# Kernel optimization log

Hardware: AMD Instinct MI355X
Metric: run time of the kernel (lower is better)

## Reference

```python
import jax, jax.numpy as jnp
import numpy as np

B, IN, HID, H = 8192, 1024, 2048, 8
UP = 2 * IN          # input_size * proj_factor
HS = HID // H        # head size = 256
EPS = 1e-5


def _blockdiag(x, w, b):
    # x: [B, UP] -> chunk into H blocks of UP//H, per-block linear to HID//H
    xb = x.reshape(B, H, UP // H)
    y = jnp.einsum('bhi,hio->bho', xb, w)
    return y.reshape(B, HID) + b


def setup_inputs() -> dict:
    key = jax.random.key(0)
    ks = jax.random.split(key, 20)
    rn = lambda k, s: jax.random.normal(k, s, jnp.float32)
    p = lambda k, *s: rn(k, s) * 0.02
    return dict(
        x=rn(ks[0], (B, IN)),
        h_prev=rn(ks[1], (B, HID)), c_prev=rn(ks[2], (B, HID)),
        n_prev=rn(ks[3], (B, HID)), m_prev=rn(ks[4], (B, HID)),
        ln_g=jnp.ones(IN), ln_b=jnp.zeros(IN),
        w_ul=p(ks[5], IN, UP), b_ul=jnp.zeros(UP),
        w_ur=p(ks[6], IN, HID), b_ur=jnp.zeros(HID),
        conv_w=p(ks[7], 4), conv_b=jnp.zeros(()),
        w_skip=p(ks[8], UP, HID), b_skip=jnp.zeros(HID),
        w_q=p(ks[9], H, UP // H, HID // H), b_q=jnp.zeros(HID),
        w_k=p(ks[10], H, UP // H, HID // H), b_k=jnp.zeros(HID),
        w_v=p(ks[11], H, UP // H, HID // H), b_v=jnp.zeros(HID),
        w_i=p(ks[12], UP, HID), b_i=jnp.zeros(HID),
        w_f=p(ks[13], UP, HID), b_f=jnp.zeros(HID),
        w_o=p(ks[14], UP, HID), b_o=jnp.zeros(HID),
        gn_g=jnp.ones(HID), gn_b=jnp.zeros(HID),
        w_down=p(ks[15], HID, IN), b_down=jnp.zeros(IN),
    )


def reference(x, h_prev, c_prev, n_prev, m_prev, ln_g, ln_b,
              w_ul, b_ul, w_ur, b_ur, conv_w, conv_b, w_skip, b_skip,
              w_q, b_q, w_k, b_k, w_v, b_v, w_i, b_i, w_f, b_f, w_o, b_o,
              gn_g, gn_b, w_down, b_down):
    # LayerNorm over features
    mu = x.mean(-1, keepdims=True)
    var = x.var(-1, keepdims=True)
    xn = (x - mu) * jax.lax.rsqrt(var + EPS) * ln_g + ln_b

    xul = xn @ w_ul + b_ul          # [B, UP]
    xur = xn @ w_ur + b_ur          # [B, HID]

    # causal conv1d (kernel 4, 1 channel) along the feature axis, left-pad 3
    xp = jnp.pad(xul, ((0, 0), (3, 0)))
    xc = conv_b + sum(conv_w[j] * xp[:, j:j + UP] for j in range(4))
    xc = jax.nn.silu(xc)            # [B, UP]

    x_skip = xc @ w_skip + b_skip

    q = _blockdiag(xc, w_q, b_q)
    k = _blockdiag(xc, w_k, b_k) / np.sqrt(HS).astype(np.float32)
    v = _blockdiag(xul, w_v, b_v)

    i_t = xc @ w_i + b_i
    f_t = xc @ w_f + b_f
    o = jax.nn.sigmoid(xul @ w_o + b_o)

    m_t = jnp.maximum(f_t + m_prev, i_t)
    i = jnp.exp(i_t - m_t)
    f = jnp.exp(f_t + m_prev - m_t)
    c_t = f * c_prev + i * (v * k)
    n_t = f * n_prev + i * k

    denom = jnp.max(jnp.abs(n_t.T @ q), axis=1)     # [HID]
    h_t = o * (c_t * q) / denom

    # GroupNorm on (N, C), groups = H
    hg = h_t.reshape(B, H, HID // H)
    gm = hg.mean(-1, keepdims=True)
    gv = hg.var(-1, keepdims=True)
    hn = ((hg - gm) * jax.lax.rsqrt(gv + EPS)).reshape(B, HID) * gn_g + gn_b

    out = (hn + x_skip) * jax.nn.silu(xur)
    return out @ w_down + b_down + x, h_t, c_t, n_t, m_t
```

## Files before the change

kernel.cpp:

```cpp
#include <hip/hip_runtime.h>
#include <stdint.h>

#define B_    8192
#define IN_   1024
#define HID_  2048
#define UP_   2048
#define H_    8
#define HS_   256
#define EPS_  1e-5f

typedef __bf16 bf16x8 __attribute__((ext_vector_type(8)));
typedef float f32x4 __attribute__((ext_vector_type(4)));
typedef unsigned short u16x4 __attribute__((ext_vector_type(4)));
typedef unsigned short u16x8 __attribute__((ext_vector_type(8)));

__device__ __forceinline__ unsigned short f2bf(float f) {
  union { float f; unsigned int u; } v; v.f = f;
  unsigned int u = v.u;
  unsigned int r = (u + 0x7fffu + ((u >> 16) & 1u)) >> 16;
  return (unsigned short)r;
}
__device__ __forceinline__ float bf2f(unsigned short h) {
  union { unsigned int u; float f; } v; v.u = ((unsigned int)h) << 16;
  return v.f;
}

__device__ __forceinline__ void gload_lds16(const void* g, void* l) {
  auto gp = reinterpret_cast<const uint32_t __attribute__((address_space(1)))*>(
      reinterpret_cast<uintptr_t>(g));
  auto lp = reinterpret_cast<uint32_t __attribute__((address_space(3)))*>(
      reinterpret_cast<uintptr_t>(l));
  __builtin_amdgcn_global_load_lds(gp, lp, 16, 0, 0);
}

template <typename OutT, bool HAS_ADD>
__global__ __launch_bounds__(512, 2) void gemm8p(
    const unsigned short* __restrict__ A, int lda, int a_zoff,
    const unsigned short* __restrict__ W, int ldw, int w_zoff,
    const float* __restrict__ bias, int bias_zoff,
    OutT* __restrict__ C, int ldc, int c_zoff,
    const float* __restrict__ ADD, float scale, int K)
{
  __shared__ char lds[131072];
  const int z = blockIdx.z;
  A += (size_t)z * a_zoff;
  W += (size_t)z * w_zoff;
  if (bias) bias += (size_t)z * bias_zoff;

  const int nwg = gridDim.x * gridDim.y;
  const int orig = blockIdx.y * gridDim.x + blockIdx.x;
  const int q8 = nwg >> 3, r8 = nwg & 7;
  const int xcd = orig & 7, xi = orig >> 3;
  const int wg = (xcd < r8 ? xcd * (q8 + 1) : r8 * (q8 + 1) + (xcd - r8) * q8) + xi;
  const int bx = wg % gridDim.x, by = wg / gridDim.x;

  const int t = threadIdx.x;
  const int lane = t & 63, wave = t >> 6;
  const int wr = wave >> 2, wc = wave & 3;
  const int l15 = lane & 15, l4 = lane >> 4;
  const int row0 = by * 256, col0 = bx * 256;

  const int lrow = lane >> 3;
  const int lslot = (lane & 7) ^ lrow;
  const size_t aLane = (size_t)lrow * lda * 2 + (size_t)lslot * 16;
  const size_t wLane = (size_t)lrow * ldw * 2 + (size_t)lslot * 16;
  const char* Abase = (const char*)A;
  const char* Wbase = (const char*)W;

  const int aRdBase = (wr * 128 + l15) * 128 + (((l4) ^ (l15 & 7)) * 16);
  const int bRdBase = (wc * 64 + l15) * 128 + (((l4) ^ (l15 & 7)) * 16);

  auto issueA = [&](int buf, int half, int tile) {
#pragma unroll
    for (int j = 0; j < 2; ++j) {
      const int rbase = half * 128 + j * 64 + wave * 8;
      gload_lds16(Abase + (size_t)(row0 + rbase) * (lda * 2) + (size_t)tile * 128 + aLane,
                  lds + buf * 65536 + rbase * 128 + lane * 16);
    }
  };
  auto issueB = [&](int buf, int half, int tile) {
#pragma unroll
    for (int j = 0; j < 2; ++j) {
      const int rbase = half * 128 + j * 64 + wave * 8;
      gload_lds16(Wbase + (size_t)(col0 + rbase) * (ldw * 2) + (size_t)tile * 128 + wLane,
                  lds + buf * 65536 + 32768 + rbase * 128 + lane * 16);
    }
  };

  f32x4 acc[8][4] = {};
  const int NT = K >> 6;

  issueA(0, 0, 0); issueA(0, 1, 0);
  issueB(0, 0, 0); issueB(0, 1, 0);
  issueB(1, 0, 1); issueB(1, 1, 1);
  asm volatile("s_waitcnt vmcnt(4)" ::: "memory");
  __builtin_amdgcn_s_barrier();
  __builtin_amdgcn_sched_barrier(0);

  for (int T = 0; T < NT; ++T) {
    const int buf = T & 1;
    const char* ldsA = lds + buf * 65536;
    const char* ldsB = ldsA + 32768;
    bf16x8 bfr[4][2];
#pragma unroll
    for (int q = 0; q < 4; ++q) {
      if (q == 0) {
#pragma unroll
        for (int ni = 0; ni < 4; ++ni) {
          bfr[ni][0] = *(const bf16x8*)(ldsB + (bRdBase + ni * 2048));
          bfr[ni][1] = *(const bf16x8*)(ldsB + ((bRdBase + ni * 2048) ^ 64));
        }
      }
      bf16x8 af[2][2];
#pragma unroll
      for (int m2 = 0; m2 < 2; ++m2) {
        const int mi = q * 2 + m2;
        af[m2][0] = *(const bf16x8*)(ldsA + (aRdBase + mi * 2048));
        af[m2][1] = *(const bf16x8*)(ldsA + ((aRdBase + mi * 2048) ^ 64));
      }
      if (q == 0 && T + 1 < NT) issueA(buf ^ 1, 0, T + 1);
      if (q == 1 && T + 1 < NT) issueA(buf ^ 1, 1, T + 1);
      if (q == 2 && T + 2 < NT) issueB(buf, 0, T + 2);
      if (q == 3 && T + 2 < NT) issueB(buf, 1, T + 2);
      if (q == 0) asm volatile("s_waitcnt lgkmcnt(8)" ::: "memory");
      __builtin_amdgcn_s_barrier();
      asm volatile("s_waitcnt lgkmcnt(0)" ::: "memory");
      __builtin_amdgcn_sched_barrier(0);
      __builtin_amdgcn_s_setprio(1);
#pragma unroll
      for (int kq = 0; kq < 2; ++kq)
#pragma unroll
        for (int m2 = 0; m2 < 2; ++m2)
#pragma unroll
          for (int ni = 0; ni < 4; ++ni)
            acc[q * 2 + m2][ni] = __builtin_amdgcn_mfma_f32_16x16x32_bf16(
                af[m2][kq], bfr[ni][kq], acc[q * 2 + m2][ni], 0, 0, 0);
      __builtin_amdgcn_s_setprio(0);
      if (q == 3) {
        if (T + 2 < NT) asm volatile("s_waitcnt vmcnt(4)" ::: "memory");
        else            asm volatile("s_waitcnt vmcnt(0)" ::: "memory");
      }
      __builtin_amdgcn_s_barrier();
      __builtin_amdgcn_sched_barrier(0);
    }
  }

#pragma unroll
  for (int mi = 0; mi < 8; ++mi) {
#pragma unroll
    for (int ni = 0; ni < 4; ++ni) {
#pragma unroll
      for (int r = 0; r < 4; ++r) {
        const int m = row0 + wr * 128 + mi * 16 + l4 * 4 + r;
        const int n = wc * 64 + ni * 16 + l15;
        float v = acc[mi][ni][r];
        if (bias) v += bias[col0 + n];
        v *= scale;
        const size_t ci = (size_t)m * ldc + (size_t)z * c_zoff + col0 + n;
        if constexpr (HAS_ADD) v += ADD[ci];
        if constexpr (sizeof(OutT) == 2) C[ci] = (OutT)f2bf(v);
        else C[ci] = v;
      }
    }
  }
}

__global__ __launch_bounds__(256) void denom_reduce(
    const float* __restrict__ part, float* __restrict__ denom)
{
  const int m = blockIdx.x, t = threadIdx.x;
  const size_t P = (size_t)HID_ * HID_;
  float v = 0.f;
  for (int n = t; n < HID_; n += 256) {
    const size_t o = (size_t)m * HID_ + n;
    float s = part[o] + part[P + o] + part[2 * P + o] + part[3 * P + o];
    v = fmaxf(v, fabsf(s));
  }
#pragma unroll
  for (int off = 1; off < 64; off <<= 1) v = fmaxf(v, __shfl_xor(v, off, 64));
  __shared__ float red[4];
  if ((t & 63) == 0) red[t >> 6] = v;
  __syncthreads();
  if (t == 0) denom[m] = fmaxf(fmaxf(red[0], red[1]), fmaxf(red[2], red[3]));
}

template <typename InT>
__global__ __launch_bounds__(256) void transpose_bf(
    const InT* __restrict__ in, unsigned short* __restrict__ out, int R, int C)
{
  __shared__ float tile[32][33];
  const size_t zoff = (size_t)blockIdx.z * R * C;
  in += zoff; out += zoff;
  const int cb = blockIdx.x * 32, rb = blockIdx.y * 32;
  const int tx = threadIdx.x, ty = threadIdx.y;
  for (int i = ty; i < 32; i += 8) {
    InT v = in[(size_t)(rb + i) * C + cb + tx];
    float f;
    if constexpr (sizeof(InT) == 2) f = bf2f((unsigned short)v);
    else f = (float)v;
    tile[i][tx] = f;
  }
  __syncthreads();
  for (int i = ty; i < 32; i += 8)
    out[(size_t)(cb + i) * R + rb + tx] = f2bf(tile[tx][i]);
}

__global__ __launch_bounds__(256) void ln_kernel(
    const float* __restrict__ x, const float* __restrict__ g,
    const float* __restrict__ b, unsigned short* __restrict__ xn)
{
  const int brow = blockIdx.x, t = threadIdx.x;
  const int lane = t & 63, wave = t >> 6;
  const float* xr = x + (size_t)brow * IN_;
  f32x4 v = *(const f32x4*)(xr + t * 4);
  float s = v[0] + v[1] + v[2] + v[3];
  float q = v[0]*v[0] + v[1]*v[1] + v[2]*v[2] + v[3]*v[3];
#pragma unroll
  for (int off = 32; off; off >>= 1) {
    s += __shfl_xor(s, off, 64);
    q += __shfl_xor(q, off, 64);
  }
  __shared__ float ss[4], sq[4];
  if (lane == 0) { ss[wave] = s; sq[wave] = q; }
  __syncthreads();
  s = ss[0] + ss[1] + ss[2] + ss[3];
  q = sq[0] + sq[1] + sq[2] + sq[3];
  const float mean = s * (1.f / IN_);
  const float var = q * (1.f / IN_) - mean * mean;
  const float rs = rsqrtf(var + EPS_);
  u16x4 o;
#pragma unroll
  for (int e = 0; e < 4; ++e) {
    const int j = t * 4 + e;
    o[e] = f2bf((v[e] - mean) * rs * g[j] + b[j]);
  }
  *(u16x4*)(xn + (size_t)brow * IN_ + t * 4) = o;
}

__global__ __launch_bounds__(256) void conv_kernel(
    const unsigned short* __restrict__ xul, const float* __restrict__ cw,
    const float* __restrict__ cb, unsigned short* __restrict__ xc)
{
  const int brow = blockIdx.x, t = threadIdx.x;
  const size_t base = (size_t)brow * UP_;
  const int j0 = t * 8;
  float xv[11];
#pragma unroll
  for (int e = 0; e < 11; ++e) {
    const int j = j0 + e - 3;
    xv[e] = (j >= 0) ? bf2f(xul[base + j]) : 0.f;
  }
  const float w0 = cw[0], w1 = cw[1], w2 = cw[2], w3 = cw[3], bb = cb[0];
  u16x8 o;
#pragma unroll
  for (int e = 0; e < 8; ++e) {
    float sv = bb + w0 * xv[e] + w1 * xv[e + 1] + w2 * xv[e + 2] + w3 * xv[e + 3];
    o[e] = f2bf(sv / (1.f + expf(-sv)));
  }
  *(u16x8*)(xc + base + j0) = o;
}

__global__ __launch_bounds__(256) void gates_kernel(
    const float* __restrict__ it_, const float* __restrict__ ft_,
    const unsigned short* __restrict__ kb, const unsigned short* __restrict__ vb,
    const float* __restrict__ mprev, const float* __restrict__ cprev,
    const float* __restrict__ nprev,
    float* __restrict__ mo, float* __restrict__ co, float* __restrict__ no)
{
  const size_t idx = ((size_t)blockIdx.x * 256 + threadIdx.x) * 4;
  f32x4 iv = *(const f32x4*)(it_ + idx);
  f32x4 fv = *(const f32x4*)(ft_ + idx);
  f32x4 mp = *(const f32x4*)(mprev + idx);
  f32x4 cp = *(const f32x4*)(cprev + idx);
  f32x4 np = *(const f32x4*)(nprev + idx);
  u16x4 kv = *(const u16x4*)(kb + idx);
  u16x4 vv = *(const u16x4*)(vb + idx);
  f32x4 mo4, co4, no4;
#pragma unroll
  for (int e = 0; e < 4; ++e) {
    const float ft = fv[e] + mp[e];
    const float mt = fmaxf(ft, iv[e]);
    const float ie = expf(iv[e] - mt);
    const float fe = expf(ft - mt);
    const float k = bf2f(kv[e]), v = bf2f(vv[e]);
    mo4[e] = mt;
    co4[e] = fe * cp[e] + ie * (v * k);
    no4[e] = fe * np[e] + ie * k;
  }
  *(f32x4*)(mo + idx) = mo4;
  *(f32x4*)(co + idx) = co4;
  *(f32x4*)(no + idx) = no4;
}

__global__ __launch_bounds__(256) void hgn_kernel(
    const float* __restrict__ ct, const unsigned short* __restrict__ olin,
    const unsigned short* __restrict__ qb, const float* __restrict__ denom,
    const unsigned short* __restrict__ skipb, const unsigned short* __restrict__ xurb,
    const float* __restrict__ gng, const float* __restrict__ gnb,
    float* __restrict__ ho, unsigned short* __restrict__ pre)
{
  const int brow = blockIdx.x, t = threadIdx.x;
  const size_t base = (size_t)brow * HID_ + t * 8;
  u16x8 ov = *(const u16x8*)(olin + base);
  u16x8 qv = *(const u16x8*)(qb + base);
  f32x4 c0 = *(const f32x4*)(ct + base);
  f32x4 c1 = *(const f32x4*)(ct + base + 4);
  float h[8];
  float s = 0.f, sq = 0.f;
#pragma unroll
  for (int e = 0; e < 8; ++e) {
    const float o = 1.f / (1.f + expf(-bf2f(ov[e])));
    const float cv = (e < 4) ? c0[e] : c1[e - 4];
    const float hv = o * cv * bf2f(qv[e]) / denom[t * 8 + e];
    h[e] = hv; s += hv; sq += hv * hv;
  }
#pragma unroll
  for (int e = 0; e < 8; ++e) ho[base + e] = h[e];
#pragma unroll
  for (int off = 1; off < 32; off <<= 1) {
    s += __shfl_xor(s, off, 64);
    sq += __shfl_xor(sq, off, 64);
  }
  const float mean = s * (1.f / HS_);
  const float var = sq * (1.f / HS_) - mean * mean;
  const float rs = rsqrtf(var + EPS_);
  u16x8 sv = *(const u16x8*)(skipb + base);
  u16x8 xv = *(const u16x8*)(xurb + base);
  u16x8 pv;
#pragma unroll
  for (int e = 0; e < 8; ++e) {
    const int j = t * 8 + e;
    const float hn = (h[e] - mean) * rs * gng[j] + gnb[j];
    const float xr = bf2f(xv[e]);
    const float sil = xr / (1.f + expf(-xr));
    pv[e] = f2bf((hn + bf2f(sv[e])) * sil);
  }
  *(u16x8*)(pre + base) = pv;
}

extern "C" void kernel_launch(void* const* d_in, const int* in_sizes, int n_in,
                              void* d_out, int out_size, void* d_ws, size_t ws_size,
                              hipStream_t stream)
{
  const float* x      = (const float*)d_in[0];
  const float* c_prev = (const float*)d_in[2];
  const float* n_prev = (const float*)d_in[3];
  const float* m_prev = (const float*)d_in[4];
  const float* ln_g   = (const float*)d_in[5];
  const float* ln_b   = (const float*)d_in[6];
  const float* w_ul   = (const float*)d_in[7];
  const float* b_ul   = (const float*)d_in[8];
  const float* w_ur   = (const float*)d_in[9];
  const float* b_ur   = (const float*)d_in[10];
  const float* conv_w = (const float*)d_in[11];
  const float* conv_b = (const float*)d_in[12];
  const float* w_skip = (const float*)d_in[13];
  const float* b_skip = (const float*)d_in[14];
  const float* w_q    = (const float*)d_in[15];
  const float* b_q    = (const float*)d_in[16];
  const float* w_k    = (const float*)d_in[17];
  const float* b_k    = (const float*)d_in[18];
  const float* w_v    = (const float*)d_in[19];
  const float* b_v    = (const float*)d_in[20];
  const float* w_i    = (const float*)d_in[21];
  const float* b_i    = (const float*)d_in[22];
  const float* w_f    = (const float*)d_in[23];
  const float* b_f    = (const float*)d_in[24];
  const float* w_o    = (const float*)d_in[25];
  const float* b_o    = (const float*)d_in[26];
  const float* gn_g   = (const float*)d_in[27];
  const float* gn_b   = (const float*)d_in[28];
  const float* w_down = (const float*)d_in[29];
  const float* b_down = (const float*)d_in[30];

  float* out_p = (float*)d_out;
  float* h_p = out_p + (size_t)B_ * IN_;
  float* c_p = h_p + (size_t)B_ * HID_;
  float* n_p = c_p + (size_t)B_ * HID_;
  float* m_p = n_p + (size_t)B_ * HID_;

  char* ws = (char*)d_ws;
  size_t off = 0;
  auto alloc = [&](size_t n) -> void* {
    void* p = ws + off;
    off += (n + 255) & ~(size_t)255;
    return p;
  };

  const size_t BH2 = (size_t)B_ * HID_ * 2;
  const size_t BH4 = (size_t)B_ * HID_ * 4;

  unsigned short* xn_bf   = (unsigned short*)alloc((size_t)B_ * IN_ * 2);
  unsigned short* xul_bf  = (unsigned short*)alloc(BH2);
  unsigned short* xur_bf  = (unsigned short*)alloc(BH2);
  unsigned short* xc_bf   = (unsigned short*)alloc(BH2);
  unsigned short* skip_bf = (unsigned short*)alloc(BH2);
  unsigned short* q_bf    = (unsigned short*)alloc(BH2);
  unsigned short* k_bf    = (unsigned short*)alloc(BH2);
  unsigned short* v_bf    = (unsigned short*)alloc(BH2);
  unsigned short* olin_bf = (unsigned short*)alloc(BH2);
  unsigned short* qT_bf   = (unsigned short*)alloc(BH2);
  unsigned short* nT_bf   = (unsigned short*)alloc(BH2);
  unsigned short* pre_bf  = (unsigned short*)alloc(BH2);
  float* i_f   = (float*)alloc(BH4);
  float* f_f   = (float*)alloc(BH4);
  float* denom = (float*)alloc(HID_ * sizeof(float));
  float* part  = (float*)alloc((size_t)4 * HID_ * HID_ * sizeof(float));
  unsigned short* wt_ul   = (unsigned short*)alloc((size_t)IN_ * UP_ * 2);
  unsigned short* wt_ur   = (unsigned short*)alloc((size_t)IN_ * HID_ * 2);
  unsigned short* wt_skip = (unsigned short*)alloc((size_t)UP_ * HID_ * 2);
  unsigned short* wt_q    = (unsigned short*)alloc((size_t)H_ * HS_ * HS_ * 2);
  unsigned short* wt_k    = (unsigned short*)alloc((size_t)H_ * HS_ * HS_ * 2);
  unsigned short* wt_v    = (unsigned short*)alloc((size_t)H_ * HS_ * HS_ * 2);
  unsigned short* wt_i    = (unsigned short*)alloc((size_t)UP_ * HID_ * 2);
  unsigned short* wt_f    = (unsigned short*)alloc((size_t)UP_ * HID_ * 2);
  unsigned short* wt_o    = (unsigned short*)alloc((size_t)UP_ * HID_ * 2);
  unsigned short* wt_down = (unsigned short*)alloc((size_t)HID_ * IN_ * 2);

  if (off > ws_size) return;

  const dim3 tb32(32, 8);

  transpose_bf<float><<<dim3(64, 32, 1), tb32, 0, stream>>>(w_ul, wt_ul, 1024, 2048);
  transpose_bf<float><<<dim3(64, 32, 1), tb32, 0, stream>>>(w_ur, wt_ur, 1024, 2048);
  transpose_bf<float><<<dim3(64, 64, 1), tb32, 0, stream>>>(w_skip, wt_skip, 2048, 2048);
  transpose_bf<float><<<dim3(8, 8, 8), tb32, 0, stream>>>(w_q, wt_q, 256, 256);
  transpose_bf<float><<<dim3(8, 8, 8), tb32, 0, stream>>>(w_k, wt_k, 256, 256);
  transpose_bf<float><<<dim3(8, 8, 8), tb32, 0, stream>>>(w_v, wt_v, 256, 256);
  transpose_bf<float><<<dim3(64, 64, 1), tb32, 0, stream>>>(w_i, wt_i, 2048, 2048);
  transpose_bf<float><<<dim3(64, 64, 1), tb32, 0, stream>>>(w_f, wt_f, 2048, 2048);
  transpose_bf<float><<<dim3(64, 64, 1), tb32, 0, stream>>>(w_o, wt_o, 2048, 2048);
  transpose_bf<float><<<dim3(32, 64, 1), tb32, 0, stream>>>(w_down, wt_down, 2048, 1024);

  ln_kernel<<<B_, 256, 0, stream>>>(x, ln_g, ln_b, xn_bf);

  gemm8p<unsigned short, false><<<dim3(8, 32, 1), 512, 0, stream>>>(
      xn_bf, IN_, 0, wt_ul, IN_, 0, b_ul, 0, xul_bf, UP_, 0, nullptr, 1.f, IN_);
  gemm8p<unsigned short, false><<<dim3(8, 32, 1), 512, 0, stream>>>(
      xn_bf, IN_, 0, wt_ur, IN_, 0, b_ur, 0, xur_bf, HID_, 0, nullptr, 1.f, IN_);

  conv_kernel<<<B_, 256, 0, stream>>>(xul_bf, conv_w, conv_b, xc_bf);

  gemm8p<unsigned short, false><<<dim3(8, 32, 1), 512, 0, stream>>>(
      xc_bf, UP_, 0, wt_skip, UP_, 0, b_skip, 0, skip_bf, HID_, 0, nullptr, 1.f, UP_);
  gemm8p<unsigned short, false><<<dim3(1, 32, 8), 512, 0, stream>>>(
      xc_bf, UP_, HS_, wt_q, HS_, HS_ * HS_, b_q, HS_, q_bf, HID_, HS_, nullptr, 1.f, HS_);
  gemm8p<unsigned short, false><<<dim3(1, 32, 8), 512, 0, stream>>>(
      xc_bf, UP_, HS_, wt_k, HS_, HS_ * HS_, b_k, HS_, k_bf, HID_, HS_, nullptr, 0.0625f, HS_);
  gemm8p<unsigned short, false><<<dim3(1, 32, 8), 512, 0, stream>>>(
      xul_bf, UP_, HS_, wt_v, HS_, HS_ * HS_, b_v, HS_, v_bf, HID_, HS_, nullptr, 1.f, HS_);
  gemm8p<float, false><<<dim3(8, 32, 1), 512, 0, stream>>>(
      xc_bf, UP_, 0, wt_i, UP_, 0, b_i, 0, i_f, HID_, 0, nullptr, 1.f, UP_);
  gemm8p<float, false><<<dim3(8, 32, 1), 512, 0, stream>>>(
      xc_bf, UP_, 0, wt_f, UP_, 0, b_f, 0, f_f, HID_, 0, nullptr, 1.f, UP_);
  gemm8p<unsigned short, false><<<dim3(8, 32, 1), 512, 0, stream>>>(
      xul_bf, UP_, 0, wt_o, UP_, 0, b_o, 0, olin_bf, HID_, 0, nullptr, 1.f, UP_);

  gates_kernel<<<(B_ * HID_ / 4) / 256, 256, 0, stream>>>(
      i_f, f_f, k_bf, v_bf, m_prev, c_prev, n_prev, m_p, c_p, n_p);

  transpose_bf<unsigned short><<<dim3(64, 256, 1), tb32, 0, stream>>>(q_bf, qT_bf, B_, HID_);
  transpose_bf<float><<<dim3(64, 256, 1), tb32, 0, stream>>>(n_p, nT_bf, B_, HID_);

  gemm8p<float, false><<<dim3(8, 8, 4), 512, 0, stream>>>(
      nT_bf, B_, HID_, qT_bf, B_, HID_, nullptr, 0,
      part, HID_, HID_ * HID_, nullptr, 1.f, B_ / 4);
  denom_reduce<<<HID_, 256, 0, stream>>>(part, denom);

  hgn_kernel<<<B_, 256, 0, stream>>>(
      c_p, olin_bf, q_bf, denom, skip_bf, xur_bf, gn_g, gn_b, h_p, pre_bf);

  gemm8p<float, true><<<dim3(4, 32, 1), 512, 0, stream>>>(
      pre_bf, UP_, 0, wt_down, UP_, 0, b_down, 0, out_p, IN_, 0, x, 1.f, UP_);
}
```

Baseline: 1.039 ms.

## Batch same-input GEMMs into wide GEMMs and fuse n transpose into gates

Several projections that share an input now run as single wider GEMMs: ul/ur share one launch, skip/i/f form one 6144-wide GEMM, and q/k share one launch, with an epilogue that routes output columns to separate buffers, biases and scales. The i and f gate pre-activations are now stored in bf16 instead of fp32, which cuts memory traffic but lowers precision of the exponent inputs. The gates kernel is retiled to 64x64 blocks and writes the transposed bf16 n directly through LDS, removing a separate transpose pass over n. This reduces launches and tail effects and reuses A tiles across the fused outputs.

```diff
diff --git a/kernel.cpp b/kernel.cpp
--- a/kernel.cpp
+++ b/kernel.cpp
@@ -37,15 +37,18 @@
 __global__ __launch_bounds__(512, 2) void gemm8p(
     const unsigned short* __restrict__ A, int lda, int a_zoff,
     const unsigned short* __restrict__ W, int ldw, int w_zoff,
-    const float* __restrict__ bias, int bias_zoff,
-    OutT* __restrict__ C, int ldc, int c_zoff,
-    const float* __restrict__ ADD, float scale, int K)
+    const float* __restrict__ bias, const float* __restrict__ bias2,
+    int bias_zoff,
+    OutT* __restrict__ C, OutT* __restrict__ C2, int ldc, int c_zoff,
+    int c_split,
+    const float* __restrict__ ADD, float scale, float scale2, int K)
 {
   __shared__ char lds[131072];
   const int z = blockIdx.z;
   A += (size_t)z * a_zoff;
   W += (size_t)z * w_zoff;
   if (bias) bias += (size_t)z * bias_zoff;
+  if (bias2) bias2 += (size_t)z * bias_zoff;
 
   const int nwg = gridDim.x * gridDim.y;
   const int orig = blockIdx.y * gridDim.x + blockIdx.x;
@@ -145,6 +148,11 @@
     }
   }
 
+  const float* bp = bias;
+  OutT* Cp = C;
+  int cbase = col0;
+  float sc = scale;
+  if (col0 >= c_split) { bp = bias2; Cp = C2; cbase = col0 - c_split; sc = scale2; }
 #pragma unroll
   for (int mi = 0; mi < 8; ++mi) {
 #pragma unroll
@@ -154,12 +162,12 @@
         const int m = row0 + wr * 128 + mi * 16 + l4 * 4 + r;
         const int n = wc * 64 + ni * 16 + l15;
         float v = acc[mi][ni][r];
-        if (bias) v += bias[col0 + n];
-        v *= scale;
-        const size_t ci = (size_t)m * ldc + (size_t)z * c_zoff + col0 + n;
+        if (bp) v += bp[cbase + n];
+        v *= sc;
+        const size_t ci = (size_t)m * ldc + (size_t)z * c_zoff + cbase + n;
         if constexpr (HAS_ADD) v += ADD[ci];
-        if constexpr (sizeof(OutT) == 2) C[ci] = (OutT)f2bf(v);
-        else C[ci] = v;
+        if constexpr (sizeof(OutT) == 2) Cp[ci] = (OutT)f2bf(v);
+        else Cp[ci] = v;
       }
     }
   }
@@ -186,11 +194,12 @@
 
 template <typename InT>
 __global__ __launch_bounds__(256) void transpose_bf(
-    const InT* __restrict__ in, unsigned short* __restrict__ out, int R, int C)
+    const InT* __restrict__ in, unsigned short* __restrict__ out, int R, int C,
+    int izoff, int ozoff)
 {
   __shared__ float tile[32][33];
-  const size_t zoff = (size_t)blockIdx.z * R * C;
-  in += zoff; out += zoff;
+  in += (size_t)blockIdx.z * izoff;
+  out += (size_t)blockIdx.z * ozoff;
   const int cb = blockIdx.x * 32, rb = blockIdx.y * 32;
   const int tx = threadIdx.x, ty = threadIdx.y;
   for (int i = ty; i < 32; i += 8) {
@@ -261,41 +270,65 @@
 }
 
 __global__ __launch_bounds__(256) void gates_kernel(
-    const float* __restrict__ it_, const float* __restrict__ ft_,
+    const unsigned short* __restrict__ sif,
     const unsigned short* __restrict__ kb, const unsigned short* __restrict__ vb,
     const float* __restrict__ mprev, const float* __restrict__ cprev,
     const float* __restrict__ nprev,
-    float* __restrict__ mo, float* __restrict__ co, float* __restrict__ no)
-{
-  const size_t idx = ((size_t)blockIdx.x * 256 + threadIdx.x) * 4;
-  f32x4 iv = *(const f32x4*)(it_ + idx);
-  f32x4 fv = *(const f32x4*)(ft_ + idx);
-  f32x4 mp = *(const f32x4*)(mprev + idx);
-  f32x4 cp = *(const f32x4*)(cprev + idx);
-  f32x4 np = *(const f32x4*)(nprev + idx);
-  u16x4 kv = *(const u16x4*)(kb + idx);
-  u16x4 vv = *(const u16x4*)(vb + idx);
-  f32x4 mo4, co4, no4;
-#pragma unroll
-  for (int e = 0; e < 4; ++e) {
-    const float ft = fv[e] + mp[e];
-    const float mt = fmaxf(ft, iv[e]);
-    const float ie = expf(iv[e] - mt);
-    const float fe = expf(ft - mt);
-    const float k = bf2f(kv[e]), v = bf2f(vv[e]);
-    mo4[e] = mt;
-    co4[e] = fe * cp[e] + ie * (v * k);
-    no4[e] = fe * np[e] + ie * k;
-  }
-  *(f32x4*)(mo + idx) = mo4;
-  *(f32x4*)(co + idx) = co4;
-  *(f32x4*)(no + idx) = no4;
+    float* __restrict__ mo, float* __restrict__ co, float* __restrict__ no,
+    unsigned short* __restrict__ nT)
+{
+  __shared__ unsigned short nt_t[64][72];
+  const int t = threadIdx.x;
+  const int r = t >> 2, cq = t & 3;
+  const int row = blockIdx.y * 64 + r;
+  const int colb = blockIdx.x * 64 + cq * 16;
+  const size_t hidb = (size_t)row * HID_ + colb;
+  const size_t sifb = (size_t)row * 6144 + colb;
+#pragma unroll
+  for (int e4 = 0; e4 < 4; ++e4) {
+    const int c4 = e4 * 4;
+    f32x4 mp = *(const f32x4*)(mprev + hidb + c4);
+    f32x4 cp = *(const f32x4*)(cprev + hidb + c4);
+    f32x4 np = *(const f32x4*)(nprev + hidb + c4);
+    u16x4 iv = *(const u16x4*)(sif + sifb + 2048 + c4);
+    u16x4 fv = *(const u16x4*)(sif + sifb + 4096 + c4);
+    u16x4 kv = *(const u16x4*)(kb + hidb + c4);
+    u16x4 vv = *(const u16x4*)(vb + hidb + c4);
+    f32x4 mo4, co4, no4;
+#pragma unroll
+    for (int e = 0; e < 4; ++e) {
+      const float ft = bf2f(fv[e]) + mp[e];
+      const float it = bf2f(iv[e]);
+      const float mt = fmaxf(ft, it);
+      const float ie = expf(it - mt);
+      const float fe = expf(ft - mt);
+      const float k = bf2f(kv[e]), v = bf2f(vv[e]);
+      mo4[e] = mt;
+      co4[e] = fe * cp[e] + ie * (v * k);
+      no4[e] = fe * np[e] + ie * k;
+      nt_t[r][cq * 16 + c4 + e] = f2bf(no4[e]);
+    }
+    *(f32x4*)(mo + hidb + c4) = mo4;
+    *(f32x4*)(co + hidb + c4) = co4;
+    *(f32x4*)(no + hidb + c4) = no4;
+  }
+  __syncthreads();
+  const int cT = t >> 2, sq = t & 3;
+  u16x8 o0, o1;
+#pragma unroll
+  for (int e = 0; e < 8; ++e) {
+    o0[e] = nt_t[sq * 16 + e][cT];
+    o1[e] = nt_t[sq * 16 + 8 + e][cT];
+  }
+  const size_t ob = (size_t)(blockIdx.x * 64 + cT) * B_ + blockIdx.y * 64 + sq * 16;
+  *(u16x8*)(nT + ob) = o0;
+  *(u16x8*)(nT + ob + 8) = o1;
 }
 
 __global__ __launch_bounds__(256) void hgn_kernel(
     const float* __restrict__ ct, const unsigned short* __restrict__ olin,
     const unsigned short* __restrict__ qb, const float* __restrict__ denom,
-    const unsigned short* __restrict__ skipb, const unsigned short* __restrict__ xurb,
+    const unsigned short* __restrict__ sif, const unsigned short* __restrict__ xurb,
     const float* __restrict__ gng, const float* __restrict__ gnb,
     float* __restrict__ ho, unsigned short* __restrict__ pre)
 {
@@ -324,7 +357,7 @@
   const float mean = s * (1.f / HS_);
   const float var = sq * (1.f / HS_) - mean * mean;
   const float rs = rsqrtf(var + EPS_);
-  u16x8 sv = *(const u16x8*)(skipb + base);
+  u16x8 sv = *(const u16x8*)(sif + (size_t)brow * 6144 + t * 8);
   u16x8 xv = *(const u16x8*)(xurb + base);
   u16x8 pv;
 #pragma unroll
@@ -388,13 +421,12 @@
   };
 
   const size_t BH2 = (size_t)B_ * HID_ * 2;
-  const size_t BH4 = (size_t)B_ * HID_ * 4;
 
   unsigned short* xn_bf   = (unsigned short*)alloc((size_t)B_ * IN_ * 2);
   unsigned short* xul_bf  = (unsigned short*)alloc(BH2);
   unsigned short* xur_bf  = (unsigned short*)alloc(BH2);
   unsigned short* xc_bf   = (unsigned short*)alloc(BH2);
-  unsigned short* skip_bf = (unsigned short*)alloc(BH2);
+  unsigned short* sif_bf  = (unsigned short*)alloc((size_t)B_ * 6144 * 2);
   unsigned short* q_bf    = (unsigned short*)alloc(BH2);
   unsigned short* k_bf    = (unsigned short*)alloc(BH2);
   unsigned short* v_bf    = (unsigned short*)alloc(BH2);
@@ -402,74 +434,75 @@
   unsigned short* qT_bf   = (unsigned short*)alloc(BH2);
   unsigned short* nT_bf   = (unsigned short*)alloc(BH2);
   unsigned short* pre_bf  = (unsigned short*)alloc(BH2);
-  float* i_f   = (float*)alloc(BH4);
-  float* f_f   = (float*)alloc(BH4);
   float* denom = (float*)alloc(HID_ * sizeof(float));
   float* part  = (float*)alloc((size_t)4 * HID_ * HID_ * sizeof(float));
-  unsigned short* wt_ul   = (unsigned short*)alloc((size_t)IN_ * UP_ * 2);
-  unsigned short* wt_ur   = (unsigned short*)alloc((size_t)IN_ * HID_ * 2);
-  unsigned short* wt_skip = (unsigned short*)alloc((size_t)UP_ * HID_ * 2);
-  unsigned short* wt_q    = (unsigned short*)alloc((size_t)H_ * HS_ * HS_ * 2);
-  unsigned short* wt_k    = (unsigned short*)alloc((size_t)H_ * HS_ * HS_ * 2);
+  float* b_sif = (float*)alloc(6144 * sizeof(float));
+  unsigned short* wt_ulur = (unsigned short*)alloc((size_t)4096 * IN_ * 2);
+  unsigned short* wt_sif  = (unsigned short*)alloc((size_t)6144 * UP_ * 2);
+  unsigned short* wt_qk   = (unsigned short*)alloc((size_t)H_ * 512 * HS_ * 2);
   unsigned short* wt_v    = (unsigned short*)alloc((size_t)H_ * HS_ * HS_ * 2);
-  unsigned short* wt_i    = (unsigned short*)alloc((size_t)UP_ * HID_ * 2);
-  unsigned short* wt_f    = (unsigned short*)alloc((size_t)UP_ * HID_ * 2);
   unsigned short* wt_o    = (unsigned short*)alloc((size_t)UP_ * HID_ * 2);
   unsigned short* wt_down = (unsigned short*)alloc((size_t)HID_ * IN_ * 2);
 
   if (off > ws_size) return;
 
   const dim3 tb32(32, 8);
-
-  transpose_bf<float><<<dim3(64, 32, 1), tb32, 0, stream>>>(w_ul, wt_ul, 1024, 2048);
-  transpose_bf<float><<<dim3(64, 32, 1), tb32, 0, stream>>>(w_ur, wt_ur, 1024, 2048);
-  transpose_bf<float><<<dim3(64, 64, 1), tb32, 0, stream>>>(w_skip, wt_skip, 2048, 2048);
-  transpose_bf<float><<<dim3(8, 8, 8), tb32, 0, stream>>>(w_q, wt_q, 256, 256);
-  transpose_bf<float><<<dim3(8, 8, 8), tb32, 0, stream>>>(w_k, wt_k, 256, 256);
-  transpose_bf<float><<<dim3(8, 8, 8), tb32, 0, stream>>>(w_v, wt_v, 256, 256);
-  transpose_bf<float><<<dim3(64, 64, 1), tb32, 0, stream>>>(w_i, wt_i, 2048, 2048);
-  transpose_bf<float><<<dim3(64, 64, 1), tb32, 0, stream>>>(w_f, wt_f, 2048, 2048);
-  transpose_bf<float><<<dim3(64, 64, 1), tb32, 0, stream>>>(w_o, wt_o, 2048, 2048);
-  transpose_bf<float><<<dim3(32, 64, 1), tb32, 0, stream>>>(w_down, wt_down, 2048, 1024);
+  const int NOSPLIT = 1 << 30;
+
+  hipMemcpyAsync(b_sif, b_skip, 2048 * 4, hipMemcpyDeviceToDevice, stream);
+  hipMemcpyAsync(b_sif + 2048, b_i, 2048 * 4, hipMemcpyDeviceToDevice, stream);
+  hipMemcpyAsync(b_sif + 4096, b_f, 2048 * 4, hipMemcpyDeviceToDevice, stream);
+
+  transpose_bf<float><<<dim3(64, 32, 1), tb32, 0, stream>>>(w_ul, wt_ulur, 1024, 2048, 0, 0);
+  transpose_bf<float><<<dim3(64, 32, 1), tb32, 0, stream>>>(w_ur, wt_ulur + (size_t)2048 * 1024, 1024, 2048, 0, 0);
+  transpose_bf<float><<<dim3(64, 64, 1), tb32, 0, stream>>>(w_skip, wt_sif, 2048, 2048, 0, 0);
+  transpose_bf<float><<<dim3(64, 64, 1), tb32, 0, stream>>>(w_i, wt_sif + (size_t)2048 * 2048, 2048, 2048, 0, 0);
+  transpose_bf<float><<<dim3(64, 64, 1), tb32, 0, stream>>>(w_f, wt_sif + (size_t)4096 * 2048, 2048, 2048, 0, 0);
+  transpose_bf<float><<<dim3(8, 8, 8), tb32, 0, stream>>>(w_q, wt_qk, 256, 256, 65536, 131072);
+  transpose_bf<float><<<dim3(8, 8, 8), tb32, 0, stream>>>(w_k, wt_qk + 65536, 256, 256, 65536, 131072);
+  transpose_bf<float><<<dim3(8, 8, 8), tb32, 0, stream>>>(w_v, wt_v, 256, 256, 65536, 65536);
+  transpose_bf<float><<<dim3(64, 64, 1), tb32, 0, stream>>>(w_o, wt_o, 2048, 2048, 0, 0);
+  transpose_bf<float><<<dim3(32, 64, 1), tb32, 0, stream>>>(w_down, wt_down, 2048, 1024, 0, 0);
 
   ln_kernel<<<B_, 256, 0, stream>>>(x, ln_g, ln_b, xn_bf);
 
+  gemm8p<unsigned short, false><<<dim3(16, 32, 1), 512, 0, stream>>>(
+      xn_bf, IN_, 0, wt_ulur, IN_, 0, b_ul, b_ur, 0,
+      xul_bf, xur_bf, HID_, 0, 2048, nullptr, 1.f, 1.f, IN_);
+
+  conv_kernel<<<B_, 256, 0, stream>>>(xul_bf, conv_w, conv_b, xc_bf);
+
+  gemm8p<unsigned short, false><<<dim3(24, 32, 1), 512, 0, stream>>>(
+      xc_bf, UP_, 0, wt_sif, UP_, 0, b_sif, nullptr, 0,
+      sif_bf, sif_bf, 6144, 0, NOSPLIT, nullptr, 1.f, 1.f, UP_);
+
+  gemm8p<unsigned short, false><<<dim3(2, 32, 8), 512, 0, stream>>>(
+      xc_bf, UP_, HS_, wt_qk, HS_, 512 * HS_, b_q, b_k, HS_,
+      q_bf, k_bf, HID_, HS_, 256, nullptr, 1.f, 0.0625f, HS_);
+
+  gemm8p<unsigned short, false><<<dim3(1, 32, 8), 512, 0, stream>>>(
+      xul_bf, UP_, HS_, wt_v, HS_, HS_ * HS_, b_v, nullptr, HS_,
+      v_bf, v_bf, HID_, HS_, NOSPLIT, nullptr, 1.f, 1.f, HS_);
+
   gemm8p<unsigned short, false><<<dim3(8, 32, 1), 512, 0, stream>>>(
-      xn_bf, IN_, 0, wt_ul, IN_, 0, b_ul, 0, xul_bf, UP_, 0, nullptr, 1.f, IN_);
-  gemm8p<unsigned short, false><<<dim3(8, 32, 1), 512, 0, stream>>>(
-      xn_bf, IN_, 0, wt_ur, IN_, 0, b_ur, 0, xur_bf, HID_, 0, nullptr, 1.f, IN_);
-
-  conv_kernel<<<B_, 256, 0, stream>>>(xul_bf, conv_w, conv_b, xc_bf);
-
-  gemm8p<unsigned short, false><<<dim3(8, 32, 1), 512, 0, stream>>>(
-      xc_bf, UP_, 0, wt_skip, UP_, 0, b_skip, 0, skip_bf, HID_, 0, nullptr, 1.f, UP_);
-  gemm8p<unsigned short, false><<<dim3(1, 32, 8), 512, 0, stream>>>(
-      xc_bf, UP_, HS_, wt_q, HS_, HS_ * HS_, b_q, HS_, q_bf, HID_, HS_, nullptr, 1.f, HS_);
-  gemm8p<unsigned short, false><<<dim3(1, 32, 8), 512, 0, stream>>>(
-      xc_bf, UP_, HS_, wt_k, HS_, HS_ * HS_, b_k, HS_, k_bf, HID_, HS_, nullptr, 0.0625f, HS_);
-  gemm8p<unsigned short, false><<<dim3(1, 32, 8), 512, 0, stream>>>(
-      xul_bf, UP_, HS_, wt_v, HS_, HS_ * HS_, b_v, HS_, v_bf, HID_, HS_, nullptr, 1.f, HS_);
-  gemm8p<float, false><<<dim3(8, 32, 1), 512, 0, stream>>>(
-      xc_bf, UP_, 0, wt_i, UP_, 0, b_i, 0, i_f, HID_, 0, nullptr, 1.f, UP_);
-  gemm8p<float, false><<<dim3(8, 32, 1), 512, 0, stream>>>(
-      xc_bf, UP_, 0, wt_f, UP_, 0, b_f, 0, f_f, HID_, 0, nullptr, 1.f, UP_);
-  gemm8p<unsigned short, false><<<dim3(8, 32, 1), 512, 0, stream>>>(
-      xul_bf, UP_, 0, wt_o, UP_, 0, b_o, 0, olin_bf, HID_, 0, nullptr, 1.f, UP_);
-
-  gates_kernel<<<(B_ * HID_ / 4) / 256, 256, 0, stream>>>(
-      i_f, f_f, k_bf, v_bf, m_prev, c_prev, n_prev, m_p, c_p, n_p);
-
-  transpose_bf<unsigned short><<<dim3(64, 256, 1), tb32, 0, stream>>>(q_bf, qT_bf, B_, HID_);
-  transpose_bf<float><<<dim3(64, 256, 1), tb32, 0, stream>>>(n_p, nT_bf, B_, HID_);
+      xul_bf, UP_, 0, wt_o, UP_, 0, b_o, nullptr, 0,
+      olin_bf, olin_bf, HID_, 0, NOSPLIT, nullptr, 1.f, 1.f, UP_);
+
+  gates_kernel<<<dim3(HID_ / 64, B_ / 64, 1), 256, 0, stream>>>(
+      sif_bf, k_bf, v_bf, m_prev, c_prev, n_prev, m_p, c_p, n_p, nT_bf);
+
+  transpose_bf<unsigned short><<<dim3(64, 256, 1), tb32, 0, stream>>>(
+      q_bf, qT_bf, B_, HID_, 0, 0);
 
   gemm8p<float, false><<<dim3(8, 8, 4), 512, 0, stream>>>(
-      nT_bf, B_, HID_, qT_bf, B_, HID_, nullptr, 0,
-      part, HID_, HID_ * HID_, nullptr, 1.f, B_ / 4);
+      nT_bf, B_, B_ / 4, qT_bf, B_, B_ / 4, nullptr, nullptr, 0,
+      part, part, HID_, HID_ * HID_, NOSPLIT, nullptr, 1.f, 1.f, B_ / 4);
   denom_reduce<<<HID_, 256, 0, stream>>>(part, denom);
 
   hgn_kernel<<<B_, 256, 0, stream>>>(
-      c_p, olin_bf, q_bf, denom, skip_bf, xur_bf, gn_g, gn_b, h_p, pre_bf);
+      c_p, olin_bf, q_bf, denom, sif_bf, xur_bf, gn_g, gn_b, h_p, pre_bf);
 
   gemm8p<float, true><<<dim3(4, 32, 1), 512, 0, stream>>>(
-      pre_bf, UP_, 0, wt_down, UP_, 0, b_down, 0, out_p, IN_, 0, x, 1.f, UP_);
-}
+      pre_bf, UP_, 0, wt_down, UP_, 0, b_down, nullptr, 0,
+      out_p, out_p, IN_, 0, NOSPLIT, x, 1.f, 1.f, UP_);
+}
```

Result: slower. 1.076 ms (+3.6%).
